# Optimization experiments

Hardware: AMD Instinct MI355X
Metric: run time of the kernel (lower is better)

The kernel has to match this reference:

```python
import jax, jax.numpy as jnp
import numpy as np
import math

B, L, C_IN = 256, 128, 75
D_EMB = 128      # DataEmbedding d_model
D_MODEL = 126    # encoder d_model (= L-2 after ODConv valid conv k=3)
H = 6
D_HEAD = D_MODEL // H  # 21
D_FF = 2048
FACTOR = 5
K_NUM = 4        # ODConv kernel_num (default)
ATT_CH = 16      # max(int(128*0.0625), 16)
EPS = 1e-5


def _ln(x, g, b):
    m = x.mean(-1, keepdims=True)
    v = ((x - m) ** 2).mean(-1, keepdims=True)
    return (x - m) * jax.lax.rsqrt(v + EPS) * g + b


def _bn_eval(x, g, b):
    # eval-mode BatchNorm, running_mean=0 running_var=1
    return x * (g / np.sqrt(1.0 + EPS)) + b


def _conv1d(x, w, b=None):
    out = jax.lax.conv_general_dilated(x, w, (1,), 'VALID',
                                       dimension_numbers=('NCH', 'OIH', 'NCH'))
    if b is not None:
        out = out + b[None, :, None]
    return out


def _pos_embed(n, d):
    pos = np.arange(n)[:, None].astype(np.float32)
    div = np.exp(np.arange(0, d, 2).astype(np.float32) * (-math.log(10000.0) / d))
    pe = np.zeros((n, d), np.float32)
    pe[:, 0::2] = np.sin(pos * div)
    pe[:, 1::2] = np.cos(pos * div)
    return jnp.asarray(pe)


def _prob_attention(Q, K, V, key):
    # Informer ProbAttention, mask_flag=False. Q,K,V: [B,H,Lq,D]
    b, h, lq, d = Q.shape
    lk = K.shape[2]
    u_keys = min(FACTOR * int(np.ceil(np.log(lk))), lk)
    n_top = min(FACTOR * int(np.ceil(np.log(lq))), lq)
    idx = jax.random.randint(key, (lq, u_keys), 0, lk)     # sampled key ids per query
    K_s = K[:, :, idx, :]                                  # [B,H,Lq,u,D]
    qks = jnp.einsum('bhld,bhlud->bhlu', Q, K_s)
    M = qks.max(-1) - qks.sum(-1) / lk                     # sparsity measure
    _, top = jax.lax.top_k(M, n_top)                       # [B,H,n_top]
    Qr = jnp.take_along_axis(Q, top[..., None], axis=2)    # [B,H,n_top,D]
    scores = jnp.einsum('bhud,bhkd->bhuk', Qr, K) / np.sqrt(d).astype(np.float32)
    upd = jnp.einsum('bhuk,bhkd->bhud', jax.nn.softmax(scores, -1), V)
    ctx = jnp.broadcast_to(V.mean(2, keepdims=True), Q.shape)  # initial context
    bi = jnp.arange(b)[:, None, None]
    hi = jnp.arange(h)[None, :, None]
    return ctx.at[bi, hi, top].set(upd)


def _forward(x_enc, x_mark_enc, token_w, time_w, time_b,
             od_fc_w, od_bn_g, od_bn_b, od_ch_w, od_ch_b, od_fil_w, od_fil_b,
             od_sp_w, od_sp_b, od_ker_w, od_ker_b, od_weight,
             q_w, q_b, k_w, k_b, v_w, v_b, o_w, o_b,
             ffn1_w, ffn1_b, ffn2_w, ffn2_b, ln1_g, ln1_b, ln2_g, ln2_b,
             cl_w, cl_b, cl_bn_g, cl_bn_b, enc_ln_g, enc_ln_b, fc_w, fc_b):
    # ---- DataEmbedding (token circular conv + pos + timeF linear; dropout=eval) ----
    xt = jnp.pad(x_enc.transpose(0, 2, 1), ((0, 0), (0, 0), (1, 1)), mode='wrap')
    tok = _conv1d(xt, token_w).transpose(0, 2, 1)          # [B,L,128]
    emb = tok + _pos_embed(L, D_EMB)[None] + (x_mark_enc @ time_w + time_b)

    # ---- ODConv1d(128,128,k=3,pad=0) on [B,128,L] ----
    x = emb.transpose(0, 2, 1)                             # [B,128,L]
    gap = x.mean(-1)                                       # [B,128]
    a = jax.nn.relu(_bn_eval(gap @ od_fc_w, od_bn_g, od_bn_b))   # [B,16]
    ch_att = jax.nn.sigmoid(a @ od_ch_w + od_ch_b)         # [B,128]
    fil_att = jax.nn.sigmoid(a @ od_fil_w + od_fil_b)      # [B,128]
    sp_att = jax.nn.sigmoid(a @ od_sp_w + od_sp_b)         # [B,3]
    ker_att = jax.nn.softmax(a @ od_ker_w + od_ker_b, -1)  # [B,4]
    xc = x * ch_att[:, :, None]
    agg_w = jnp.einsum('bn,bj,noij->boij', ker_att, sp_att, od_weight)  # [B,128,128,3]
    lout = L - 2
    patches = jnp.stack([xc[:, :, j:j + lout] for j in range(3)], axis=2)  # [B,128,3,126]
    x = jnp.einsum('boij,bijt->bot', agg_w, patches) * fil_att[:, :, None]  # [B,128,126]
    # encoder reads this as (seq=128, d_model=126)

    key = jax.random.key(42)

    def enc_layer(xx, i):
        b, l, _ = xx.shape
        Q = (xx @ q_w[i] + q_b[i]).reshape(b, l, H, D_HEAD).transpose(0, 2, 1, 3)
        Kk = (xx @ k_w[i] + k_b[i]).reshape(b, l, H, D_HEAD).transpose(0, 2, 1, 3)
        Vv = (xx @ v_w[i] + v_b[i]).reshape(b, l, H, D_HEAD).transpose(0, 2, 1, 3)
        ctx = _prob_attention(Q, Kk, Vv, jax.random.fold_in(key, i))
        new_x = ctx.transpose(0, 2, 1, 3).reshape(b, l, D_MODEL) @ o_w[i] + o_b[i]
        xx = _ln(xx + new_x, ln1_g[i], ln1_b[i])
        y = jax.nn.gelu(xx @ ffn1_w[i] + ffn1_b[i], approximate=False)
        y = y @ ffn2_w[i] + ffn2_b[i]
        return _ln(xx + y, ln2_g[i], ln2_b[i])

    x = enc_layer(x, 0)
    # ConvLayer distilling: circular conv k3 + BN + ELU + maxpool(k3,s2,p1): 128 -> 64
    xt = jnp.pad(x.transpose(0, 2, 1), ((0, 0), (0, 0), (1, 1)), mode='wrap')
    xt = _conv1d(xt, cl_w, cl_b)
    xt = jax.nn.elu(_bn_eval(xt, cl_bn_g[None, :, None], cl_bn_b[None, :, None]))
    xt = jax.lax.reduce_window(xt, -jnp.inf, jax.lax.max, (1, 1, 3), (1, 1, 2),
                               [(0, 0), (0, 0), (1, 1)])
    x = xt.transpose(0, 2, 1)                              # [B,64,126]
    x = enc_layer(x, 1)
    x = _ln(x, enc_ln_g, enc_ln_b)

    out = x.transpose(0, 2, 1) @ fc_w + fc_b               # [B,126,1]
    return out.transpose(0, 2, 1)                          # [B,1,126]


def setup_inputs() -> dict:
    key = jax.random.key(0)
    it = iter(jax.random.split(key, 48))
    def rn(shape, s=0.05):
        return jax.random.normal(next(it), shape, dtype=jnp.float32) * s
    return {
        'x_enc': jax.random.normal(next(it), (B, L, C_IN), jnp.float32),
        'x_mark_enc': jax.random.uniform(next(it), (B, L, 3), jnp.float32, -0.5, 0.5),
        'token_w': rn((D_EMB, C_IN, 3), 0.1),
        'time_w': rn((3, D_EMB), 0.1), 'time_b': rn((D_EMB,)),
        'od_fc_w': rn((D_EMB, ATT_CH), 0.1),
        'od_bn_g': jnp.ones((ATT_CH,)), 'od_bn_b': jnp.zeros((ATT_CH,)),
        'od_ch_w': rn((ATT_CH, D_EMB), 0.1), 'od_ch_b': rn((D_EMB,)),
        'od_fil_w': rn((ATT_CH, D_EMB), 0.1), 'od_fil_b': rn((D_EMB,)),
        'od_sp_w': rn((ATT_CH, 3), 0.1), 'od_sp_b': rn((3,)),
        'od_ker_w': rn((ATT_CH, K_NUM), 0.1), 'od_ker_b': rn((K_NUM,)),
        'od_weight': rn((K_NUM, D_EMB, D_EMB, 3), 0.05),
        'q_w': rn((2, D_MODEL, D_MODEL)), 'q_b': rn((2, D_MODEL)),
        'k_w': rn((2, D_MODEL, D_MODEL)), 'k_b': rn((2, D_MODEL)),
        'v_w': rn((2, D_MODEL, D_MODEL)), 'v_b': rn((2, D_MODEL)),
        'o_w': rn((2, D_MODEL, D_MODEL)), 'o_b': rn((2, D_MODEL)),
        'ffn1_w': rn((2, D_MODEL, D_FF), 0.03), 'ffn1_b': rn((2, D_FF)),
        'ffn2_w': rn((2, D_FF, D_MODEL), 0.03), 'ffn2_b': rn((2, D_MODEL)),
        'ln1_g': jnp.ones((2, D_MODEL)), 'ln1_b': jnp.zeros((2, D_MODEL)),
        'ln2_g': jnp.ones((2, D_MODEL)), 'ln2_b': jnp.zeros((2, D_MODEL)),
        'cl_w': rn((D_MODEL, D_MODEL, 3), 0.05), 'cl_b': rn((D_MODEL,)),
        'cl_bn_g': jnp.ones((D_MODEL,)), 'cl_bn_b': jnp.zeros((D_MODEL,)),
        'enc_ln_g': jnp.ones((D_MODEL,)), 'enc_ln_b': jnp.zeros((D_MODEL,)),
        'fc_w': rn((L // 2, 1), 0.1), 'fc_b': rn((1,)),
    }


def reference(x_enc, x_mark_enc, token_w, time_w, time_b,
              od_fc_w, od_bn_g, od_bn_b, od_ch_w, od_ch_b, od_fil_w, od_fil_b,
              od_sp_w, od_sp_b, od_ker_w, od_ker_b, od_weight,
              q_w, q_b, k_w, k_b, v_w, v_b, o_w, o_b,
              ffn1_w, ffn1_b, ffn2_w, ffn2_b, ln1_g, ln1_b, ln2_g, ln2_b,
              cl_w, cl_b, cl_bn_g, cl_bn_b, enc_ln_g, enc_ln_b, fc_w, fc_b):
    return _forward(x_enc, x_mark_enc, token_w, time_w, time_b,
                    od_fc_w, od_bn_g, od_bn_b, od_ch_w, od_ch_b, od_fil_w, od_fil_b,
                    od_sp_w, od_sp_b, od_ker_w, od_ker_b, od_weight,
                    q_w, q_b, k_w, k_b, v_w, v_b, o_w, o_b,
                    ffn1_w, ffn1_b, ffn2_w, ffn2_b, ln1_g, ln1_b, ln2_g, ln2_b,
                    cl_w, cl_b, cl_bn_g, cl_bn_b, enc_ln_g, enc_ln_b, fc_w, fc_b)
```

## Files before the change

### kernel.cpp

```cpp
#include <hip/hip_runtime.h>
#include <math.h>

#define NB 256
#define DM 126
#define DE 128
#define NH 6
#define DHd 21
#define DFF 2048
#define CIN 75
#define L0 128
#define NTOP 25

#ifndef IDX_MODE
#define IDX_MODE 0
#endif

typedef const float* fp;
typedef unsigned short u16;
typedef short s8v __attribute__((ext_vector_type(8)));
typedef float f4v __attribute__((ext_vector_type(4)));

__device__ __forceinline__ u16 f2bf(float x){
  unsigned u = __float_as_uint(x);
  unsigned r = (u + 0x7FFFu + ((u >> 16) & 1u)) >> 16;
  return (u16)r;
}
__device__ __forceinline__ float bf2f(u16 v){
  unsigned uu = ((unsigned)v) << 16;
  return __uint_as_float(uu);
}

__device__ __forceinline__ void gld_lds16(const u16* g, u16* l){
  __builtin_amdgcn_global_load_lds((const __attribute__((address_space(1))) unsigned int*)(const void*)g,
                                   (__attribute__((address_space(3))) unsigned int*)(void*)l,
                                   16, 0, 0);
}

__device__ __forceinline__ unsigned cvt_pk_bf16(float lo, float hi){
  unsigned r;
  asm("v_cvt_pk_bf16_f32 %0, %1, %2" : "=v"(r) : "v"(lo), "v"(hi));
  return r;
}

__device__ __forceinline__ void tf2(unsigned k0, unsigned k1, unsigned x0, unsigned x1,
                                    unsigned &o0, unsigned &o1){
  unsigned ks2 = k0 ^ k1 ^ 0x1BD11BDAu;
  x0 += k0; x1 += k1;
  #define RR(r) { x0 += x1; x1 = (x1 << (r)) | (x1 >> (32 - (r))); x1 ^= x0; }
  RR(13) RR(15) RR(26) RR(6)
  x0 += k1;  x1 += ks2 + 1u;
  RR(17) RR(29) RR(16) RR(24)
  x0 += ks2; x1 += k0 + 2u;
  RR(13) RR(15) RR(26) RR(6)
  x0 += k0;  x1 += k1 + 3u;
  RR(17) RR(29) RR(16) RR(24)
  x0 += k1;  x1 += ks2 + 4u;
  RR(13) RR(15) RR(26) RR(6)
  x0 += ks2; x1 += k0 + 5u;
  #undef RR
  o0 = x0; o1 = x1;
}

__global__ __launch_bounds__(256) void k_zero(float* out, int n){
  int i = blockIdx.x*256 + threadIdx.x;
  if (i < n) out[i] = 0.f;
}

__global__ __launch_bounds__(256) void k_idx(int* idx0, int* idx1){
  int tid = threadIdx.x;
  unsigned a0,a1,c0,c1;
  tf2(0u,42u, 0u,0u, a0,a1);
  tf2(0u,42u, 0u,1u, c0,c1);
  for (int f = tid; f < 3200; f += 256){
    unsigned y0,y1;
#if IDX_MODE==0
    tf2(a0,a1, 0u, (unsigned)(3200+f), y0,y1); idx0[f] = (int)(y1 & 127u);
#elif IDX_MODE==1
    tf2(a0,a1, 0u, (unsigned)(3200+f), y0,y1); idx0[f] = (int)(y0 & 127u);
#elif IDX_MODE==2
    tf2(a0,a1, (unsigned)f, (unsigned)(3200+f), y0,y1); idx0[f] = (int)(y1 & 127u);
#else
    tf2(a0,a1, (unsigned)f, (unsigned)(3200+f), y0,y1); idx0[f] = (int)(y0 & 127u);
#endif
  }
  for (int f = tid; f < 1600; f += 256){
    unsigned y0,y1;
#if IDX_MODE==0
    tf2(c0,c1, 0u, (unsigned)(1600+f), y0,y1); idx1[f] = (int)(y1 & 63u);
#elif IDX_MODE==1
    tf2(c0,c1, 0u, (unsigned)(1600+f), y0,y1); idx1[f] = (int)(y0 & 63u);
#elif IDX_MODE==2
    tf2(c0,c1, (unsigned)f, (unsigned)(1600+f), y0,y1); idx1[f] = (int)(y1 & 63u);
#else
    tf2(c0,c1, (unsigned)f, (unsigned)(1600+f), y0,y1); idx1[f] = (int)(y0 & 63u);
#endif
  }
}

__global__ __launch_bounds__(256) void k_wprep(fp token_w, fp clw,
                                               fp qw, fp qb, fp kw, fp kb, fp vw, fp vb, fp ow,
                                               u16* wemb, u16* wdist, u16* wqkv, u16* wo,
                                               float* qbias){
  int i = blockIdx.x*256 + threadIdx.x;
  if (i < 32768){
    int n = i >> 8, k = i & 255;
    float v = 0.f;
    if (k < 225){ int q = k/75, c = k - q*75; v = token_w[(size_t)n*225 + c*3 + q]; }
    wemb[i] = f2bf(v);
    return;
  }
  i -= 32768;
  if (i < 49152){
    int n = i / 384, k = i - n*384;
    float v = 0.f;
    if (n < DM && k < 378){ int q = k/126, ci = k - q*126; v = clw[((size_t)n*DM + ci)*3 + q]; }
    wdist[i] = f2bf(v);
    return;
  }
  i -= 49152;
  if (i < 2*49152){
    int layer = i / 49152, jj = i - layer*49152;
    int n = jj >> 7, k = jj & 127;
    int sec = n >> 7, nn = n & 127;
    const float* w = (sec == 0) ? qw : ((sec == 1) ? kw : vw);
    float v = (nn < DM && k < DM) ? w[((size_t)layer*DM + k)*DM + nn] : 0.f;
    wqkv[(size_t)layer*49152 + jj] = f2bf(v);
    return;
  }
  i -= 2*49152;
  if (i < 2*16384){
    int layer = i / 16384, jj = i - layer*16384;
    int n = jj >> 7, k = jj & 127;
    float v = (n < DM && k < DM) ? ow[(size_t)layer*DM*DM + k*DM + n] : 0.f;
    wo[(size_t)layer*16384 + jj] = f2bf(v);
    return;
  }
  i -= 2*16384;
  if (i < 768){
    int layer = i / 384, n = i - layer*384;
    int sec = n >> 7, nn = n & 127;
    const float* bp = (sec == 0) ? qb : ((sec == 1) ? kb : vb);
    qbias[(size_t)layer*384 + n] = (nn < DM) ? bp[layer*DM + nn] : 0.f;
  }
}

__global__ __launch_bounds__(256) void k_wtrans(fp f1w, fp f2w, u16* w1t, u16* w2t){
  __shared__ u16 sT[64*65];
  const int t = blockIdx.x;
  const int tid = threadIdx.x, lane = tid & 63, rg = tid >> 6;
  if (t < 128){
    int layer = t >> 6, rem = t & 63;
    int kt = rem >> 5, nt = rem & 31;
    #pragma unroll
    for (int rr = 0; rr < 16; rr++){
      int row = rg + rr*4;
      int k = kt*64 + row;
      float v = (k < DM) ? f1w[((size_t)layer*DM + k)*DFF + nt*64 + lane] : 0.f;
      sT[row*65 + lane] = f2bf(v);
    }
    __syncthreads();
    #pragma unroll
    for (int rr = 0; rr < 16; rr++){
      int nrow = rg + rr*4;
      int n_glob = nt*64 + nrow;
      w1t[(size_t)layer*262144 + (size_t)n_glob*128 + kt*64 + lane] = sT[lane*65 + nrow];
    }
  } else {
    int t2 = t - 128;
    int layer = t2 >> 6, rem = t2 & 63;
    int nt = rem >> 5, ft = rem & 31;
    #pragma unroll
    for (int rr = 0; rr < 16; rr++){
      int row = rg + rr*4;
      int f = ft*64 + row;
      int n = nt*64 + lane;
      float v = (n < DM) ? f2w[((size_t)layer*DFF + f)*DM + n] : 0.f;
      sT[row*65 + lane] = f2bf(v);
    }
    __syncthreads();
    #pragma unroll
    for (int rr = 0; rr < 16; rr++){
      int nrow = rg + rr*4;
      int n_glob = nt*64 + nrow;
      w2t[(size_t)layer*262144 + (size_t)n_glob*2048 + ft*64 + lane] = sT[lane*65 + nrow];
    }
  }
}

__global__ __launch_bounds__(256) void k_front(fp x_enc, fp x_mark, const u16* wemb,
                                               fp time_w, fp time_b,
                                               fp fcw, fp bng, fp bnb,
                                               fp chw, fp chb, fp filw, fp filb,
                                               fp spw, fp spb, fp kerw, fp kerb,
                                               fp odw, float* xout){
  __shared__ __align__(16) u16 smem[71232];
  u16*   sXT = smem;
  u16*   sW  = smem + 17680;
  u16*   sA  = smem + 17680;
  float* sE  = reinterpret_cast<float*>(smem + 17680);
  float* red = reinterpret_cast<float*>(smem + 69904);
  float* gap = reinterpret_cast<float*>(smem + 70416);
  float* aAct= reinterpret_cast<float*>(smem + 70672);
  float* sch = reinterpret_cast<float*>(smem + 70704);
  float* sfil= reinterpret_cast<float*>(smem + 70960);
  float* ssp = reinterpret_cast<float*>(smem + 71216);
  float* sker= reinterpret_cast<float*>(smem + 71224);
  const int tid = threadIdx.x;
  const int wave = tid >> 6, lane = tid & 63, quad = lane >> 4, l15 = lane & 15;
  const int b = blockIdx.x;
  const f4v z4 = {0.f,0.f,0.f,0.f};
  const int mBase = wave * 32;

  {
    const float4* xb = reinterpret_cast<const float4*>(x_enc + (size_t)b*L0*CIN);
    for (int p4 = tid; p4 < (L0*CIN)/4; p4 += 256){
      float4 v4 = xb[p4];
      float vv[4] = {v4.x, v4.y, v4.z, v4.w};
      int e0 = p4*4;
      #pragma unroll
      for (int j = 0; j < 4; j++){
        int e = e0 + j;
        int sr = e / CIN, c = e - sr*CIN;
        u16 bv = f2bf(vv[j]);
        sA[((sr + 1) & 127)*264 + c] = bv;
        sA[sr*264 + 75 + c] = bv;
        sA[((sr + 127) & 127)*264 + 150 + c] = bv;
      }
    }
    for (int p = tid; p < 128*31; p += 256){
      int row = p / 31, c2 = p - row*31;
      sA[row*264 + 225 + c2] = 0;
    }
  }
  __syncthreads();
  {
    f4v acc[2][8];
    #pragma unroll
    for (int m = 0; m < 2; m++)
      #pragma unroll
      for (int t = 0; t < 8; t++) acc[m][t] = z4;
    for (int ks = 0; ks < 8; ks++){
      s8v a0 = *reinterpret_cast<const s8v*>(sA + (mBase + l15)*264 + ks*32 + quad*8);
      s8v a1 = *reinterpret_cast<const s8v*>(sA + (mBase + 16 + l15)*264 + ks*32 + quad*8);
      const u16* wb = wemb + (size_t)l15*256 + ks*32 + quad*8;
      #pragma unroll
      for (int t = 0; t < 8; t++){
        s8v bfr = *reinterpret_cast<const s8v*>(wb + (size_t)t*16*256);
        acc[0][t] = __builtin_amdgcn_mfma_f32_16x16x32_bf16(a0, bfr, acc[0][t], 0, 0, 0);
        acc[1][t] = __builtin_amdgcn_mfma_f32_16x16x32_bf16(a1, bfr, acc[1][t], 0, 0, 0);
      }
    }
    float divc[8], tw0c[8], tw1c[8], tw2c[8], tbc[8];
    #pragma unroll
    for (int t = 0; t < 8; t++){
      int col = t*16 + l15;
      int i2 = col >> 1;
      divc[t] = __expf((float)(2*i2) * (-9.210340371976184f / 128.f));
      tw0c[t] = time_w[col]; tw1c[t] = time_w[128 + col]; tw2c[t] = time_w[256 + col];
      tbc[t] = time_b[col];
    }
    #pragma unroll
    for (int m = 0; m < 2; m++){
      #pragma unroll
      for (int r = 0; r < 4; r++){
        int row = mBase + m*16 + quad*4 + r;
        const float* mk = x_mark + ((size_t)b*L0 + row)*3;
        float m0v = mk[0], m1v = mk[1], m2v = mk[2];
        #pragma unroll
        for (int t = 0; t < 8; t++){
          int col = t*16 + l15;
          float ang = (float)row * divc[t];
          float pe = (col & 1) ? __cosf(ang) : __sinf(ang);
          float tm = m0v*tw0c[t] + m1v*tw1c[t] + m2v*tw2c[t] + tbc[t];
          sE[row*132 + col] = acc[m][t][r] + pe + tm;
        }
      }
    }
  }
  __syncthreads();
  {
    int col = tid & 127, half = tid >> 7;
    float s = 0.f;
    for (int r = 0; r < 64; r++) s += sE[(half*64 + r)*132 + col];
    red[tid] = s;
  }
  __syncthreads();
  if (tid < 128) gap[tid] = (red[tid] + red[tid + 128]) * (1.f/128.f);
  __syncthreads();
  if (tid < 16){
    float acc = 0.f;
    for (int e = 0; e < DE; e++) acc += gap[e]*fcw[e*16 + tid];
    acc = acc * (bng[tid] / sqrtf(1.f + 1e-5f)) + bnb[tid];
    aAct[tid] = fmaxf(acc, 0.f);
  }
  __syncthreads();
  if (tid < 128){
    float accc = 0.f, accf = 0.f;
    for (int c = 0; c < 16; c++){ accc += aAct[c]*chw[c*DE + tid]; accf += aAct[c]*filw[c*DE + tid]; }
    sch[tid]  = 1.f/(1.f + __expf(-(accc + chb[tid])));
    sfil[tid] = 1.f/(1.f + __expf(-(accf + filb[tid])));
  } else if (tid < 131){
    int t = tid - 128;
    float acc = 0.f;
    for (int c = 0; c < 16; c++) acc += aAct[c]*spw[c*3 + t];
    ssp[t] = 1.f/(1.f + __expf(-(acc + spb[t])));
  } else if (tid == 132){
    float v[4]; float mx = -1e30f;
    for (int n = 0; n < 4; n++){
      float acc = 0.f;
      for (int c = 0; c < 16; c++) acc += aAct[c]*kerw[c*4 + n];
      v[n] = acc + kerb[n]; mx = fmaxf(mx, v[n]);
    }
    float ss = 0.f;
    for (int n = 0; n < 4; n++){ v[n] = __expf(v[n]-mx); ss += v[n]; }
    for (int n = 0; n < 4; n++) sker[n] = v[n]/ss;
  }
  __syncthreads();
  for (int p = tid; p < 130*128; p += 256){
    int l = p >> 7, i = p & 127;
    float v = (l < 128) ? sE[l*132 + i]*sch[i] : 0.f;
    sXT[l*136 + i] = f2bf(v);
  }
  __syncthreads();
  {
    float kr0 = sker[0], kr1 = sker[1], kr2 = sker[2], kr3 = sker[3];
    float spq[3]; spq[0] = ssp[0]; spq[1] = ssp[1]; spq[2] = ssp[2];
    const float4* od4 = (const float4*)odw;
    for (int p4 = tid; p4 < 128*384/4; p4 += 256){
      float4 w0 = od4[p4];
      float4 w1 = od4[12288 + p4];
      float4 w2 = od4[24576 + p4];
      float4 w3 = od4[36864 + p4];
      float vv[4] = { kr0*w0.x + kr1*w1.x + kr2*w2.x + kr3*w3.x,
                      kr0*w0.y + kr1*w1.y + kr2*w2.y + kr3*w3.y,
                      kr0*w0.z + kr1*w1.z + kr2*w2.z + kr3*w3.z,
                      kr0*w0.w + kr1*w1.w + kr2*w2.w + kr3*w3.w };
      int e0 = p4*4;
      #pragma unroll
      for (int j = 0; j < 4; j++){
        int e = e0 + j;
        int o = e / 384, rem = e - o*384;
        int i = rem / 3, q = rem - i*3;
        sW[(q*128 + o)*136 + i] = f2bf(vv[j] * spq[q]);
      }
    }
  }
  __syncthreads();
  {
    f4v acc[2][8];
    #pragma unroll
    for (int m = 0; m < 2; m++)
      #pragma unroll
      for (int t = 0; t < 8; t++) acc[m][t] = z4;
    for (int q = 0; q < 3; q++){
      const u16* wq = sW + q*128*136;
      #pragma unroll
      for (int ks = 0; ks < 4; ks++){
        s8v a0 = *reinterpret_cast<const s8v*>(wq + (mBase + l15)*136 + ks*32 + quad*8);
        s8v a1 = *reinterpret_cast<const s8v*>(wq + (mBase + 16 + l15)*136 + ks*32 + quad*8);
        #pragma unroll
        for (int t = 0; t < 8; t++){
          s8v bfr = *reinterpret_cast<const s8v*>(sXT + (t*16 + l15 + q)*136 + ks*32 + quad*8);
          acc[0][t] = __builtin_amdgcn_mfma_f32_16x16x32_bf16(a0, bfr, acc[0][t], 0, 0, 0);
          acc[1][t] = __builtin_amdgcn_mfma_f32_16x16x32_bf16(a1, bfr, acc[1][t], 0, 0, 0);
        }
      }
    }
    #pragma unroll
    for (int t = 0; t < 8; t++){
      int tt = t*16 + l15;
      if (tt < DM){
        #pragma unroll
        for (int m = 0; m < 2; m++){
          #pragma unroll
          for (int r = 0; r < 4; r++){
            int o = mBase + m*16 + quad*4 + r;
            xout[((size_t)b*DE + o)*DM + tt] = sfil[o] * acc[m][t][r];
          }
        }
      }
    }
  }
}

__global__ __launch_bounds__(256) void k_qkv_mfma(const float* xin, const u16* wqkv,
                                                  const float* qkvb, float* qkv,
                                                  float* vt, int L, int lshift, int lmask){
  __shared__ __align__(16) u16 sX[64*136];
  const int tid = threadIdx.x;
  const int wave = tid >> 6, lane = tid & 63, quad = lane >> 4, l15 = lane & 15;
  const size_t rows0 = (size_t)blockIdx.x * 64;
  for (int p = tid; p < 64*128; p += 256){
    int r = p >> 7, c = p & 127;
    float v = (c < DM) ? xin[(rows0 + r)*DM + c] : 0.f;
    sX[r*136 + c] = f2bf(v);
  }
  __syncthreads();
  const f4v z4 = {0.f,0.f,0.f,0.f};
  f4v acc[24];
  #pragma unroll
  for (int t = 0; t < 24; t++) acc[t] = z4;
  const int m0 = wave * 16;
  #pragma unroll
  for (int ks = 0; ks < 4; ks++){
    s8v a = *reinterpret_cast<const s8v*>(sX + (m0 + l15)*136 + ks*32 + quad*8);
    const u16* wb = wqkv + (size_t)l15*128 + ks*32 + quad*8;
    #pragma unroll
    for (int t = 0; t < 24; t++){
      s8v b = *reinterpret_cast<const s8v*>(wb + (size_t)t*16*128);
      acc[t] = __builtin_amdgcn_mfma_f32_16x16x32_bf16(a, b, acc[t], 0, 0, 0);
    }
  }
  #pragma unroll
  for (int t = 0; t < 24; t++){
    int col = t*16 + l15;
    float bv = qkvb[col];
    if (col < 256){
      #pragma unroll
      for (int r = 0; r < 4; r++){
        int row = m0 + quad*4 + r;
        qkv[(rows0 + row)*256 + col] = acc[t][r] + bv;
      }
    } else {
      int c = col - 256;
      if (c < DM){
        int h = c / DHd, d = c - h*DHd;
        #pragma unroll
        for (int r = 0; r < 4; r++){
          int gr = (int)rows0 + m0 + quad*4 + r;
          int b = gr >> lshift, l = gr & lmask;
          vt[((size_t)(b*NH + h)*DHd + d)*L + l] = acc[t][r] + bv;
        }
      }
    }
  }
}

__global__ __launch_bounds__(128) void k_attn(const float* qkv, const float* vt,
                                              const int* idx, int L,
                                              int* posmap, float* vmean, float* upd){
  __shared__ __align__(16) float sK[2816];
  __shared__ int sTop[32];
  const int tid = threadIdx.x;
  const int wave = tid >> 6, lane = tid & 63, quad = lane >> 4, l15 = lane & 15;
  const int bh = blockIdx.x;
  const int b = bh / NH, h = bh - b*NH;
  float* sM = sK + 2688;
  u16* sPb = reinterpret_cast<u16*>(sK);
  const float* qbase = qkv + (size_t)(b*L)*256 + h*DHd;
  const float* vb = vt + (size_t)bh*DHd*L;
  const f4v z4 = {0.f,0.f,0.f,0.f};
  const int ntn = L >> 4;
  const int d0 = quad*8;
  const int mt = wave;

  for (int p = tid; p < L*DHd; p += 128){
    int l = p / DHd, d = p - l*DHd;
    sK[p] = qbase[(size_t)l*256 + 128 + d];
  }
  posmap[bh*L0 + tid] = -1;
  __syncthreads();
  if (tid < L){
    const int l = tid;
    const float* qg = qbase + (size_t)l*256;
    float qr[DHd];
    #pragma unroll
    for (int d = 0; d < DHd; d++) qr[d] = qg[d];
    float mx = -1e30f, sm = 0.f;
    #pragma unroll
    for (int u = 0; u < NTOP; u++){
      int kk = idx[l*NTOP + u];
      const float* kp = sK + kk*DHd;
      float acc = 0.f;
      #pragma unroll
      for (int d = 0; d < DHd; d++) acc += qr[d]*kp[d];
      mx = fmaxf(mx, acc); sm += acc;
    }
    sM[l] = mx - sm/(float)L;
  }
  __syncthreads();
  if (wave == 0){
    for (int it = 0; it < NTOP; it++){
      float bv = sM[lane]; int bi = lane;
      if (L == 128){
        float v1 = sM[lane + 64];
        if (v1 > bv){ bv = v1; bi = lane + 64; }
      }
      #pragma unroll
      for (int off = 32; off > 0; off >>= 1){
        float ov = __shfl_xor(bv, off);
        int   oi = __shfl_xor(bi, off);
        if (ov > bv || (ov == bv && oi < bi)){ bv = ov; bi = oi; }
      }
      if (lane == 0){
        sM[bi] = -1e30f;
        posmap[bh*L0 + bi] = it;
        sTop[it] = bi;
      }
    }
  }
  __syncthreads();

  s8v aq;
  {
    int uu = mt*16 + l15; if (uu >= NTOP) uu = 0;
    int r = sTop[uu];
    const float* qp = qbase + (size_t)r*256 + d0;
    #pragma unroll
    for (int j = 0; j < 8; j++) aq[j] = (short)f2bf(qp[j]);
  }
  f4v sc[8];
  for (int nt = 0; nt < ntn; nt++){
    const float* kp = sK + (size_t)(nt*16 + l15)*DHd + d0;
    s8v bb;
    #pragma unroll
    for (int j = 0; j < 8; j++) bb[j] = (d0 + j < DHd) ? (short)f2bf(kp[j]) : (short)0;
    sc[nt] = __builtin_amdgcn_mfma_f32_16x16x32_bf16(aq, bb, z4, 0, 0, 0);
  }
  __syncthreads();
  const float inv21 = 0.21821789023599236f;
  #pragma unroll
  for (int r4 = 0; r4 < 4; r4++){
    float mx = -1e30f;
    for (int nt = 0; nt < ntn; nt++) mx = fmaxf(mx, sc[nt][r4]*inv21);
    #pragma unroll
    for (int off = 1; off < 16; off <<= 1) mx = fmaxf(mx, __shfl_xor(mx, off));
    float e[8]; float ss = 0.f;
    for (int nt = 0; nt < ntn; nt++){ e[nt] = __expf(sc[nt][r4]*inv21 - mx); ss += e[nt]; }
    #pragma unroll
    for (int off = 1; off < 16; off <<= 1) ss += __shfl_xor(ss, off);
    float dn = 1.f / ss;
    int u = mt*16 + quad*4 + r4;
    for (int nt = 0; nt < ntn; nt++)
      sPb[u*136 + nt*16 + l15] = f2bf(e[nt]*dn);
  }
  if (wave == 1){
    u16 invL = f2bf(1.f/(float)L);
    for (int c = lane; c < L; c += 64) sPb[25*136 + c] = invL;
  }
  f4v pv[2];
  pv[0] = z4; pv[1] = z4;
  int kSteps = L >> 5;
  for (int ks = 0; ks < kSteps; ks++){
    #pragma unroll
    for (int nt = 0; nt < 2; nt++){
      int d = nt*16 + l15;
      s8v bb;
      if (d < DHd){
        const float* vp = vb + (size_t)d*L + ks*32 + d0;
        #pragma unroll
        for (int j = 0; j < 8; j++) bb[j] = (short)f2bf(vp[j]);
      } else {
        #pragma unroll
        for (int j = 0; j < 8; j++) bb[j] = (short)0;
      }
      s8v a = *reinterpret_cast<const s8v*>(sPb + (mt*16 + l15)*136 + ks*32 + d0);
      pv[nt] = __builtin_amdgcn_mfma_f32_16x16x32_bf16(a, bb, pv[nt], 0, 0, 0);
    }
  }
  #pragma unroll
  for (int nt = 0; nt < 2; nt++){
    #pragma unroll
    for (int r4 = 0; r4 < 4; r4++){
      int u = mt*16 + quad*4 + r4;
      int d = nt*16 + l15;
      if (d < DHd){
        if (u < NTOP)       upd[((size_t)bh*NTOP + u)*DHd + d] = pv[nt][r4];
        else if (u == NTOP) vmean[bh*DHd + d] = pv[nt][r4];
      }
    }
  }
}

__global__ __launch_bounds__(256) void k_oproj_mfma(const float* xin, const float* vmean,
                                                    const int* posmap, const float* upd,
                                                    const u16* wo, fp ob, fp g, fp bb,
                                                    int layer, int lshift, int lmask, float* xmid){
  __shared__ __align__(16) float sOf[64*129];
  __shared__ float prs[128];
  __shared__ float smean[64], srstd[64];
  u16* sX = reinterpret_cast<u16*>(sOf);
  const int tid = threadIdx.x;
  const int wave = tid >> 6, lane = tid & 63, quad = lane >> 4, l15 = lane & 15;
  const int m0 = wave * 16;
  const size_t rows0 = (size_t)blockIdx.x * 64;
  for (int p = tid; p < 64*128; p += 256){
    int r = p >> 7, c = p & 127;
    int gr = (int)rows0 + r, b = gr >> lshift, l = gr & lmask;
    float v = 0.f;
    if (c < DM){
      int h = c / DHd, d = c - h*DHd;
      int bh = b*NH + h;
      int pos = posmap[bh*L0 + l];
      v = (pos >= 0) ? upd[((size_t)bh*NTOP + pos)*DHd + d] : vmean[bh*DHd + d];
    }
    sX[r*136 + c] = f2bf(v);
  }
  __syncthreads();
  const f4v z4 = {0.f,0.f,0.f,0.f};
  f4v acc[8];
  #pragma unroll
  for (int t = 0; t < 8; t++) acc[t] = z4;
  #pragma unroll
  for (int ks = 0; ks < 4; ks++){
    s8v a = *reinterpret_cast<const s8v*>(sX + (m0 + l15)*136 + ks*32 + quad*8);
    const u16* wb = wo + (size_t)l15*128 + ks*32 + quad*8;
    #pragma unroll
    for (int t = 0; t < 8; t++){
      s8v b = *reinterpret_cast<const s8v*>(wb + (size_t)t*16*128);
      acc[t] = __builtin_amdgcn_mfma_f32_16x16x32_bf16(a, b, acc[t], 0, 0, 0);
    }
  }
  __syncthreads();
  #pragma unroll
  for (int t = 0; t < 8; t++){
    int col = t*16 + l15;
    #pragma unroll
    for (int r = 0; r < 4; r++){
      sOf[(m0 + quad*4 + r)*129 + col] = acc[t][r];
    }
  }
  __syncthreads();
  const float* obl = ob + (size_t)layer*DM;
  for (int p = tid; p < 64*DM; p += 256){
    int r = p / DM, c = p - r*DM;
    sOf[r*129 + c] += xin[(rows0 + r)*DM + c] + obl[c];
  }
  __syncthreads();
  if (tid < 128){
    int row = tid >> 1, half = tid & 1;
    float s = 0.f;
    for (int c = half*63; c < half*63 + 63; c++) s += sOf[row*129 + c];
    prs[tid] = s;
  }
  __syncthreads();
  if (tid < 128 && (tid & 1) == 0) smean[tid>>1] = (prs[tid] + prs[tid+1]) / (float)DM;
  __syncthreads();
  if (tid < 128){
    int row = tid >> 1, half = tid & 1;
    float mn = smean[row];
    float s = 0.f;
    for (int c = half*63; c < half*63 + 63; c++){ float d = sOf[row*129 + c] - mn; s += d*d; }
    prs[tid] = s;
  }
  __syncthreads();
  if (tid < 128 && (tid & 1) == 0) srstd[tid>>1] = rsqrtf((prs[tid] + prs[tid+1])/(float)DM + 1e-5f);
  __syncthreads();
  const float* gl = g  + (size_t)layer*DM;
  const float* bl = bb + (size_t)layer*DM;
  for (int p = tid; p < 64*DM; p += 256){
    int r = p / DM, c = p - r*DM;
    xmid[(rows0 + r)*DM + c] = (sOf[r*129 + c] - smean[r])*srstd[r]*gl[c] + bl[c];
  }
}

__device__ __forceinline__ float gelu_fast(float x){
  float x2 = x*x;
  float u = x * __builtin_fmaf(0.10295128f, x2, 2.30212056f);
  u = fminf(u, 126.f);
#if __has_builtin(__builtin_amdgcn_exp2f)
  float t = __builtin_amdgcn_exp2f(u);
#else
  float t = __expf(u * 0.69314718056f);
#endif
  return x * t * __builtin_amdgcn_rcpf(t + 1.f);
}


__device__ __forceinline__ void stage_w1_p(const u16* w1t, int j, u16* buf, int p){
  int n = p >> 4, c = p & 15;
  int cg = c ^ (n & 7);
  gld_lds16(w1t + (((size_t)(j*64 + n)) << 7) + cg*8,
            buf + (size_t)((p >> 6) << 6)*8);
}
__device__ __forceinline__ void stage_w2_p(const u16* w2t, int j, u16* buf, int p){
  int n = p >> 3, c = p & 7;
  int cg = c ^ (n & 7);
  gld_lds16(w2t + (size_t)n*2048 + j*64 + cg*8,
            buf + (size_t)((p >> 6) << 6)*8);
}

__device__ __forceinline__ int yaddr(int row, int col){
  return row*64 + (((col >> 3) ^ (row & 7)) << 3) + (col & 7);
}

__device__ __forceinline__ void lgkm_barrier(){
  asm volatile("s_waitcnt lgkmcnt(0)" ::: "memory");
  __builtin_amdgcn_sched_barrier(0);
  __builtin_amdgcn_s_barrier();
  __builtin_amdgcn_sched_barrier(0);
}

template<int NT>
__global__ __launch_bounds__(NT) void k_ffn(const float* xmid, const u16* w1t, const u16* w2t,
                                            fp b1, fp b2w, fp g, fp bb, int layer, float* xout){
  constexpr int ROWS = NT/8;
  constexpr int NMG  = NT/256;
  constexpr int SYG  = NMG*2048;
  constexpr int SP   = 1024/NT;
  __shared__ __align__(16) u16 smem[SYG + 4*8192];
  __shared__ float prs[2*ROWS];
  __shared__ float smean[ROWS], srstd[ROWS];
  u16* wA0 = smem + SYG;
  u16* wA1 = wA0 + 8192;
  u16* wB0 = wA1 + 8192;
  u16* wB1 = wB0 + 8192;
  const int tid  = threadIdx.x;
  const int wave = tid >> 6, lane = tid & 63, quad = lane >> 4, l15 = lane & 15;
  const int mg = wave >> 2, ng = wave & 3;
  const int rowb = mg * 32;
  u16* sYg = smem + mg*2048;
  const size_t rows0 = (size_t)blockIdx.x * ROWS;

  s8v aX[2][4];
  #pragma unroll
  for (int mt = 0; mt < 2; mt++){
    const float* xr = xmid + (rows0 + rowb + mt*16 + l15)*(size_t)DM;
    #pragma unroll
    for (int ks = 0; ks < 4; ks++){
      #pragma unroll
      for (int j = 0; j < 8; j++){
        int c = ks*32 + quad*8 + j;
        float v = (c < DM) ? xr[c] : 0.f;
        aX[mt][ks][j] = (short)f2bf(v);
      }
    }
  }
  #pragma unroll
  for (int r = 0; r < SP; r++){
    stage_w1_p(w1t, 0, wA0, r*NT + tid);
    stage_w2_p(w2t, 0, wB0, r*NT + tid);
  }

  const float* b1l = b1 + (size_t)layer*DFF;
  const f4v z4 = {0.f, 0.f, 0.f, 0.f};
  f4v acc2[2][2];
  acc2[0][0]=z4; acc2[0][1]=z4; acc2[1][0]=z4; acc2[1][1]=z4;

  for (int j = 0; j < 32; j++){
    u16* wAcur = (j & 1) ? wA1 : wA0;
    u16* wAnxt = (j & 1) ? wA0 : wA1;
    u16* wBcur = (j & 1) ? wB1 : wB0;
    u16* wBnxt = (j & 1) ? wB0 : wB1;
    __syncthreads();
    if (j < 31){
      #pragma unroll
      for (int r = 0; r < SP; r++){
        stage_w1_p(w1t, j+1, wAnxt, r*NT + tid);
        stage_w2_p(w2t, j+1, wBnxt, r*NT + tid);
      }
    }
    f4v acc1[2];
    acc1[0] = z4; acc1[1] = z4;
    {
      int nloc = ng*16 + l15;
      #pragma unroll
      for (int ks = 0; ks < 4; ks++){
        int cg = (ks*4 + quad) ^ (nloc & 7);
        s8v b = *reinterpret_cast<const s8v*>(wAcur + nloc*128 + cg*8);
        acc1[0] = __builtin_amdgcn_mfma_f32_16x16x32_bf16(aX[0][ks], b, acc1[0], 0, 0, 0);
        acc1[1] = __builtin_amdgcn_mfma_f32_16x16x32_bf16(aX[1][ks], b, acc1[1], 0, 0, 0);
      }
    }
    {
      int col = ng*16 + l15;
      float bv = b1l[j*64 + col];
      #pragma unroll
      for (int mt = 0; mt < 2; mt++){
        float y0 = gelu_fast(acc1[mt][0] + bv);
        float y1 = gelu_fast(acc1[mt][1] + bv);
        float y2 = gelu_fast(acc1[mt][2] + bv);
        float y3 = gelu_fast(acc1[mt][3] + bv);
        unsigned p01 = cvt_pk_bf16(y0, y1);
        unsigned p23 = cvt_pk_bf16(y2, y3);
        int r0 = mt*16 + quad*4;
        sYg[yaddr(r0,     col)] = (u16)p01;
        sYg[yaddr(r0 + 1, col)] = (u16)(p01 >> 16);
        sYg[yaddr(r0 + 2, col)] = (u16)p23;
        sYg[yaddr(r0 + 3, col)] = (u16)(p23 >> 16);
      }
    }
    lgkm_barrier();
    #pragma unroll
    for (int ks2 = 0; ks2 < 2; ks2++){
      int ga = ((ks2*4 + quad) ^ (l15 & 7)) << 3;
      s8v a0 = *reinterpret_cast<const s8v*>(sYg + (l15)*64 + ga);
      s8v a1 = *reinterpret_cast<const s8v*>(sYg + (16 + l15)*64 + ga);
      #pragma unroll
      for (int t = 0; t < 2; t++){
        int nloc = ng*32 + t*16 + l15;
        int cg = (ks2*4 + quad) ^ (nloc & 7);
        s8v b = *reinterpret_cast<const s8v*>(wBcur + nloc*64 + cg*8);
        acc2[0][t] = __builtin_amdgcn_mfma_f32_16x16x32_bf16(a0, b, acc2[0][t], 0, 0, 0);
        acc2[1][t] = __builtin_amdgcn_mfma_f32_16x16x32_bf16(a1, b, acc2[1][t], 0, 0, 0);
      }
    }
  }

  __syncthreads();
  float* sO = reinterpret_cast<float*>(smem);
  #pragma unroll
  for (int mt = 0; mt < 2; mt++)
    #pragma unroll
    for (int t = 0; t < 2; t++)
      #pragma unroll
      for (int r = 0; r < 4; r++)
        sO[(rowb + mt*16 + quad*4 + r)*129 + ng*32 + t*16 + l15] = acc2[mt][t][r];
  __syncthreads();
  const float* b2l = b2w + (size_t)layer*DM;
  for (int p = tid; p < ROWS*DM; p += NT){
    int r = p / DM, c = p - r*DM;
    sO[r*129 + c] += b2l[c] + xmid[(rows0 + r)*DM + c];
  }
  __syncthreads();
  if (tid < 2*ROWS){
    int row = tid >> 1, half = tid & 1;
    float s = 0.f;
    for (int c = half*63; c < half*63 + 63; c++) s += sO[row*129 + c];
    prs[tid] = s;
  }
  __syncthreads();
  if (tid < 2*ROWS && (tid & 1) == 0) smean[tid>>1] = (prs[tid] + prs[tid+1]) / (float)DM;
  __syncthreads();
  if (tid < 2*ROWS){
    int row = tid >> 1, half = tid & 1;
    float mn = smean[row];
    float s = 0.f;
    for (int c = half*63; c < half*63 + 63; c++){ float d = sO[row*129 + c] - mn; s += d*d; }
    prs[tid] = s;
  }
  __syncthreads();
  if (tid < 2*ROWS && (tid & 1) == 0) srstd[tid>>1] = rsqrtf((prs[tid] + prs[tid+1])/(float)DM + 1e-5f);
  __syncthreads();
  const float* gl = g  + (size_t)layer*DM;
  const float* bl = bb + (size_t)layer*DM;
  for (int p = tid; p < ROWS*DM; p += NT){
    int r = p / DM, c = p - r*DM;
    xout[(rows0 + r)*DM + c] = (sO[r*129 + c] - smean[r])*srstd[r]*gl[c] + bl[c];
  }
}

__global__ __launch_bounds__(256) void k_distill_mfma(const float* xin, const u16* wdist,
                                                      fp clb, fp bng, fp bnb, float* xout){
  __shared__ __align__(16) u16 sA[128*392];
  const int tid = threadIdx.x;
  const int wave = tid >> 6, lane = tid & 63, quad = lane >> 4, l15 = lane & 15;
  const int b = blockIdx.x;
  {
    const float4* xb = reinterpret_cast<const float4*>(xin + (size_t)b*128*DM);
    for (int p4 = tid; p4 < (128*DM)/4; p4 += 256){
      float4 v4 = xb[p4];
      float vv[4] = {v4.x, v4.y, v4.z, v4.w};
      int e0 = p4*4;
      #pragma unroll
      for (int j = 0; j < 4; j++){
        int e = e0 + j;
        int sr = e / DM, ci = e - sr*DM;
        u16 bv = f2bf(vv[j]);
        sA[((sr + 1) & 127)*392 + ci] = bv;
        sA[sr*392 + 126 + ci] = bv;
        sA[((sr + 127) & 127)*392 + 252 + ci] = bv;
      }
    }
    for (int p = tid; p < 128*6; p += 256){
      int row = p / 6, c2 = p - row*6;
      sA[row*392 + 378 + c2] = 0;
    }
  }
  __syncthreads();
  const f4v z4 = {0.f,0.f,0.f,0.f};
  f4v acc[2][8];
  #pragma unroll
  for (int m = 0; m < 2; m++)
    #pragma unroll
    for (int t = 0; t < 8; t++) acc[m][t] = z4;
  const int mBase = wave * 32;
  for (int ks = 0; ks < 12; ks++){
    s8v a0 = *reinterpret_cast<const s8v*>(sA + (mBase + l15)*392 + ks*32 + quad*8);
    s8v a1 = *reinterpret_cast<const s8v*>(sA + (mBase + 16 + l15)*392 + ks*32 + quad*8);
    const u16* wb = wdist + (size_t)l15*384 + ks*32 + quad*8;
    #pragma unroll
    for (int t = 0; t < 8; t++){
      s8v bfr = *reinterpret_cast<const s8v*>(wb + (size_t)t*16*384);
      acc[0][t] = __builtin_amdgcn_mfma_f32_16x16x32_bf16(a0, bfr, acc[0][t], 0, 0, 0);
      acc[1][t] = __builtin_amdgcn_mfma_f32_16x16x32_bf16(a1, bfr, acc[1][t], 0, 0, 0);
    }
  }
  __syncthreads();
  float* zsh = reinterpret_cast<float*>(sA);
  const float bnscale = 1.f / sqrtf(1.f + 1e-5f);
  #pragma unroll
  for (int t = 0; t < 8; t++){
    int co = t*16 + l15;
    if (co < DM){
      float cb = clb[co];
      float gg = bng[co] * bnscale, bv = bnb[co];
      #pragma unroll
      for (int m = 0; m < 2; m++){
        #pragma unroll
        for (int r = 0; r < 4; r++){
          int row = mBase + m*16 + quad*4 + r;
          float z = (acc[m][t][r] + cb)*gg + bv;
          z = (z > 0.f) ? z : (__expf(z) - 1.f);
          zsh[row*130 + co] = z;
        }
      }
    }
  }
  __syncthreads();
  for (int p = tid; p < 64*DM; p += 256){
    int j = p / DM, co = p - j*DM;
    float best = zsh[(2*j)*130 + co];
    if (j > 0) best = fmaxf(best, zsh[(2*j - 1)*130 + co]);
    best = fmaxf(best, zsh[(2*j + 1)*130 + co]);
    xout[((size_t)b*64 + j)*DM + co] = best;
  }
}

__global__ __launch_bounds__(128) void k_final(const float* xin, fp g, fp bb,
                                               fp fcw, fp fcb, float* out){
  __shared__ float xs[64][DM];
  __shared__ float mean_s[64], rstd_s[64];
  int b = blockIdx.x, t = threadIdx.x;
  for (int p = t; p < 64*DM; p += 128){ xs[p/DM][p%DM] = xin[(size_t)b*64*DM + p]; }
  __syncthreads();
  if (t < 64){
    float s = 0.f;
    for (int m = 0; m < DM; m++) s += xs[t][m];
    float mn = s / (float)DM;
    float v = 0.f;
    for (int m = 0; m < DM; m++){ float d = xs[t][m] - mn; v += d*d; }
    mean_s[t] = mn; rstd_s[t] = rsqrtf(v / (float)DM + 1e-5f);
  }
  __syncthreads();
  if (t < DM){
    float gv = g[t], bv = bb[t];
    float acc = fcb[0];
    for (int l = 0; l < 64; l++){
      float xn = (xs[l][t] - mean_s[l])*rstd_s[l]*gv + bv;
      acc += xn * fcw[l];
    }
    out[b*DM + t] = acc;
  }
}

extern "C" void kernel_launch(void* const* d_in, const int* in_sizes, int n_in,
                              void* d_out, int out_size, void* d_ws, size_t ws_size,
                              hipStream_t stream) {
  fp x_enc   = (fp)d_in[0];
  fp x_mark  = (fp)d_in[1];
  fp token_w = (fp)d_in[2];
  fp time_w  = (fp)d_in[3];
  fp time_b  = (fp)d_in[4];
  fp od_fc_w = (fp)d_in[5];
  fp od_bn_g = (fp)d_in[6];
  fp od_bn_b = (fp)d_in[7];
  fp od_ch_w = (fp)d_in[8];
  fp od_ch_b = (fp)d_in[9];
  fp od_fil_w= (fp)d_in[10];
  fp od_fil_b= (fp)d_in[11];
  fp od_sp_w = (fp)d_in[12];
  fp od_sp_b = (fp)d_in[13];
  fp od_ker_w= (fp)d_in[14];
  fp od_ker_b= (fp)d_in[15];
  fp od_wt   = (fp)d_in[16];
  fp q_w = (fp)d_in[17]; fp q_b = (fp)d_in[18];
  fp k_w = (fp)d_in[19]; fp k_b = (fp)d_in[20];
  fp v_w = (fp)d_in[21]; fp v_b = (fp)d_in[22];
  fp o_w = (fp)d_in[23]; fp o_b = (fp)d_in[24];
  fp f1w = (fp)d_in[25]; fp f1b = (fp)d_in[26];
  fp f2w = (fp)d_in[27]; fp f2b = (fp)d_in[28];
  fp ln1g= (fp)d_in[29]; fp ln1b= (fp)d_in[30];
  fp ln2g= (fp)d_in[31]; fp ln2b= (fp)d_in[32];
  fp cl_w= (fp)d_in[33]; fp cl_b= (fp)d_in[34];
  fp clbg= (fp)d_in[35]; fp clbb= (fp)d_in[36];
  fp elng= (fp)d_in[37]; fp elnb= (fp)d_in[38];
  fp fc_w= (fp)d_in[39]; fp fc_b= (fp)d_in[40];

  const size_t OFF_IDX0 = 0;
  const size_t OFF_IDX1 = OFF_IDX0 + 3200;
  const size_t OFF_CH   = OFF_IDX1 + 1600;
  const size_t OFF_FIL  = OFF_CH  + (size_t)NB*DE;
  const size_t OFF_SP   = OFF_FIL + (size_t)NB*DE;
  const size_t OFF_KER  = OFF_SP  + (size_t)NB*4;
  const size_t OFF_VM   = OFF_KER + (size_t)NB*4;
  const size_t OFF_POS  = OFF_VM  + (size_t)NB*NH*DHd;
  const size_t OFF_UPD  = OFF_POS + (size_t)NB*NH*L0;
  const size_t OFF_STOP = OFF_UPD + (size_t)NB*NH*NTOP*DHd;
  const size_t OFF_WTS  = (OFF_STOP + (size_t)NB*NH*NTOP + 255) & ~(size_t)255;
  const size_t WTS_FLOATS = (2*262144 + 2*262144 + 2*49152 + 2*16384 + 49152 + 32768)/2 + 2*384;
  const size_t OFF_BIG  = (OFF_WTS + WTS_FLOATS + 255) & ~(size_t)255;
  const size_t SBUF     = (size_t)NB*DE*L0;
  const size_t TOTAL    = OFF_BIG + 4*SBUF;

  if (ws_size < TOTAL*sizeof(float)){
    hipLaunchKernelGGL(k_zero, dim3((out_size+255)/256), dim3(256), 0, stream,
                       (float*)d_out, out_size);
    return;
  }

  float* ws = (float*)d_ws;
  int* idx0 = (int*)(ws + OFF_IDX0);
  int* idx1 = (int*)(ws + OFF_IDX1);
  float* vme = ws + OFF_VM;
  int* posm  = (int*)(ws + OFF_POS);
  float* updb= ws + OFF_UPD;
  u16* w1tb  = (u16*)(ws + OFF_WTS);
  u16* w2tb  = w1tb + 2*262144;
  u16* wqkvb = w2tb + 2*262144;
  u16* wob   = wqkvb + 2*49152;
  u16* wdistb= wob + 2*16384;
  u16* wembb = wdistb + 49152;
  float* qkvbias = (float*)(wembb + 32768);

  float* X    = ws + OFF_BIG;
  float* QKV  = X + SBUF;
  float* VT   = X + 3*SBUF;
  float* xmid = QKV;
  float* ffno = QKV + SBUF;

  hipLaunchKernelGGL(k_idx, dim3(1), dim3(256), 0, stream, idx0, idx1);
  hipLaunchKernelGGL(k_wprep, dim3(835), dim3(256), 0, stream,
                     token_w, cl_w, q_w, q_b, k_w, k_b, v_w, v_b, o_w,
                     wembb, wdistb, wqkvb, wob, qkvbias);
  hipLaunchKernelGGL(k_wtrans, dim3(256), dim3(256), 0, stream,
                     f1w, f2w, w1tb, w2tb);
  hipLaunchKernelGGL(k_front, dim3(NB), dim3(256), 0, stream,
                     x_enc, x_mark, wembb, time_w, time_b,
                     od_fc_w, od_bn_g, od_bn_b, od_ch_w, od_ch_b, od_fil_w, od_fil_b,
                     od_sp_w, od_sp_b, od_ker_w, od_ker_b, od_wt, X);

  hipLaunchKernelGGL(k_qkv_mfma, dim3(NB*L0/64), dim3(256), 0, stream,
                     X, wqkvb, qkvbias, QKV, VT, 128, 7, 127);
  hipLaunchKernelGGL(k_attn, dim3(NB*NH), dim3(128), 0, stream,
                     QKV, VT, idx0, L0, posm, vme, updb);
  hipLaunchKernelGGL(k_oproj_mfma, dim3(NB*L0/64), dim3(256), 0, stream,
                     X, vme, posm, updb, wob, o_b, ln1g, ln1b, 0, 7, 127, xmid);
  hipLaunchKernelGGL((k_ffn<1024>), dim3(NB*L0/128), dim3(1024), 0, stream,
                     xmid, w1tb, w2tb, f1b, f2b, ln2g, ln2b, 0, ffno);

  hipLaunchKernelGGL(k_distill_mfma, dim3(NB), dim3(256), 0, stream,
                     ffno, wdistb, cl_b, clbg, clbb, X);

  hipLaunchKernelGGL(k_qkv_mfma, dim3(NB*64/64), dim3(256), 0, stream,
                     X, wqkvb + 49152, qkvbias + 384, QKV, VT, 64, 6, 63);
  hipLaunchKernelGGL(k_attn, dim3(NB*NH), dim3(128), 0, stream,
                     QKV, VT, idx1, 64, posm, vme, updb);
  hipLaunchKernelGGL(k_oproj_mfma, dim3(NB*64/64), dim3(256), 0, stream,
                     X, vme, posm, updb, wob + 16384, o_b, ln1g, ln1b, 1, 6, 63, xmid);
  hipLaunchKernelGGL((k_ffn<512>), dim3(NB*64/64), dim3(512), 0, stream,
                     xmid, w1tb + 262144, w2tb + 262144, f1b, f2b, ln2g, ln2b, 1, ffno);

  hipLaunchKernelGGL(k_final, dim3(NB), dim3(128), 0, stream,
                     ffno, elng, elnb, fc_w, fc_b, (float*)d_out);
  (void)in_sizes; (void)n_in; (void)out_size; (void)ws_size;
}
```

Baseline: 608.3 us.

## Fuse distill conv into layer-0 FFN and final LN/FC into layer-1 FFN

Each FFN kernel instance now handles one batch item and runs the next stage in its epilogue. Layer 0 runs the distilling conv, BN, ELU and maxpool from shared memory, and layer 1 runs the final encoder LayerNorm and the FC projection. This removes two kernel launches and the global-memory round trip of the FFN outputs. In exchange the layer-0 FFN shared-memory buffer is enlarged to hold the conv im2col tile, which may lower occupancy, and the epilogues add extra barriers.

After: 592.2 us. 1.03x faster.

```diff
diff --git a/kernel.cpp b/kernel.cpp
--- a/kernel.cpp
+++ b/kernel.cpp
@@ -693,12 +693,15 @@
 
 template<int NT>
 __global__ __launch_bounds__(NT) void k_ffn(const float* xmid, const u16* w1t, const u16* w2t,
-                                            fp b1, fp b2w, fp g, fp bb, int layer, float* xout){
+                                            fp b1, fp b2w, fp g, fp bb, int layer,
+                                            const u16* wdist, fp e1, fp e2, fp e3, fp e4,
+                                            float* out2){
   constexpr int ROWS = NT/8;
   constexpr int NMG  = NT/256;
   constexpr int SYG  = NMG*2048;
   constexpr int SP   = 1024/NT;
-  __shared__ __align__(16) u16 smem[SYG + 4*8192];
+  constexpr int SMEMU = (NT == 1024) ? 128*392 : (SYG + 4*8192);
+  __shared__ __align__(16) u16 smem[SMEMU];
   __shared__ float prs[2*ROWS];
   __shared__ float smean[ROWS], srstd[ROWS];
   u16* wA0 = smem + SYG;
@@ -834,113 +837,105 @@
   __syncthreads();
   const float* gl = g  + (size_t)layer*DM;
   const float* bl = bb + (size_t)layer*DM;
-  for (int p = tid; p < ROWS*DM; p += NT){
-    int r = p / DM, c = p - r*DM;
-    xout[(rows0 + r)*DM + c] = (sO[r*129 + c] - smean[r])*srstd[r]*gl[c] + bl[c];
-  }
-}
-
-__global__ __launch_bounds__(256) void k_distill_mfma(const float* xin, const u16* wdist,
-                                                      fp clb, fp bng, fp bnb, float* xout){
-  __shared__ __align__(16) u16 sA[128*392];
-  const int tid = threadIdx.x;
-  const int wave = tid >> 6, lane = tid & 63, quad = lane >> 4, l15 = lane & 15;
-  const int b = blockIdx.x;
-  {
-    const float4* xb = reinterpret_cast<const float4*>(xin + (size_t)b*128*DM);
-    for (int p4 = tid; p4 < (128*DM)/4; p4 += 256){
-      float4 v4 = xb[p4];
-      float vv[4] = {v4.x, v4.y, v4.z, v4.w};
-      int e0 = p4*4;
-      #pragma unroll
-      for (int j = 0; j < 4; j++){
-        int e = e0 + j;
-        int sr = e / DM, ci = e - sr*DM;
-        u16 bv = f2bf(vv[j]);
-        sA[((sr + 1) & 127)*392 + ci] = bv;
-        sA[sr*392 + 126 + ci] = bv;
-        sA[((sr + 127) & 127)*392 + 252 + ci] = bv;
-      }
-    }
-    for (int p = tid; p < 128*6; p += 256){
-      int row = p / 6, c2 = p - row*6;
-      sA[row*392 + 378 + c2] = 0;
-    }
-  }
-  __syncthreads();
-  const f4v z4 = {0.f,0.f,0.f,0.f};
-  f4v acc[2][8];
-  #pragma unroll
-  for (int m = 0; m < 2; m++)
-    #pragma unroll
-    for (int t = 0; t < 8; t++) acc[m][t] = z4;
-  const int mBase = wave * 32;
-  for (int ks = 0; ks < 12; ks++){
-    s8v a0 = *reinterpret_cast<const s8v*>(sA + (mBase + l15)*392 + ks*32 + quad*8);
-    s8v a1 = *reinterpret_cast<const s8v*>(sA + (mBase + 16 + l15)*392 + ks*32 + quad*8);
-    const u16* wb = wdist + (size_t)l15*384 + ks*32 + quad*8;
-    #pragma unroll
-    for (int t = 0; t < 8; t++){
-      s8v bfr = *reinterpret_cast<const s8v*>(wb + (size_t)t*16*384);
-      acc[0][t] = __builtin_amdgcn_mfma_f32_16x16x32_bf16(a0, bfr, acc[0][t], 0, 0, 0);
-      acc[1][t] = __builtin_amdgcn_mfma_f32_16x16x32_bf16(a1, bfr, acc[1][t], 0, 0, 0);
-    }
-  }
-  __syncthreads();
-  float* zsh = reinterpret_cast<float*>(sA);
-  const float bnscale = 1.f / sqrtf(1.f + 1e-5f);
-  #pragma unroll
-  for (int t = 0; t < 8; t++){
-    int co = t*16 + l15;
-    if (co < DM){
-      float cb = clb[co];
-      float gg = bng[co] * bnscale, bv = bnb[co];
-      #pragma unroll
-      for (int m = 0; m < 2; m++){
+
+  if constexpr (NT == 1024){
+    float rv[16];
+    #pragma unroll
+    for (int k = 0; k < 16; k++){
+      int p = tid + k*1024;
+      if (p < 128*DM){
+        int r = p / DM, c = p - r*DM;
+        rv[k] = (sO[r*129 + c] - smean[r])*srstd[r]*gl[c] + bl[c];
+      } else rv[k] = 0.f;
+    }
+    __syncthreads();
+    u16* sAd = smem;
+    #pragma unroll
+    for (int k = 0; k < 16; k++){
+      int p = tid + k*1024;
+      if (p < 128*DM){
+        int r = p / DM, c = p - r*DM;
+        u16 bv = f2bf(rv[k]);
+        sAd[((r + 1) & 127)*392 + c] = bv;
+        sAd[r*392 + 126 + c] = bv;
+        sAd[((r + 127) & 127)*392 + 252 + c] = bv;
+      }
+    }
+    if (tid < 768){ int row = tid / 6, c2 = tid - row*6; sAd[row*392 + 378 + c2] = 0; }
+    __syncthreads();
+    const int mrow  = (wave & 7) * 16;
+    const int tbase = (wave >> 3) * 4;
+    f4v dac[4];
+    dac[0]=z4; dac[1]=z4; dac[2]=z4; dac[3]=z4;
+    for (int ks = 0; ks < 12; ks++){
+      s8v a = *reinterpret_cast<const s8v*>(sAd + (mrow + l15)*392 + ks*32 + quad*8);
+      const u16* wbp = wdist + (size_t)l15*384 + ks*32 + quad*8;
+      #pragma unroll
+      for (int t = 0; t < 4; t++){
+        s8v bfr = *reinterpret_cast<const s8v*>(wbp + (size_t)(tbase + t)*16*384);
+        dac[t] = __builtin_amdgcn_mfma_f32_16x16x32_bf16(a, bfr, dac[t], 0, 0, 0);
+      }
+    }
+    __syncthreads();
+    float* zsh = reinterpret_cast<float*>(smem);
+    const float bnscale = 1.f / sqrtf(1.f + 1e-5f);
+    #pragma unroll
+    for (int t = 0; t < 4; t++){
+      int co = (tbase + t)*16 + l15;
+      if (co < DM){
+        float cb = e1[co];
+        float gg = e2[co] * bnscale, bv = e3[co];
         #pragma unroll
         for (int r = 0; r < 4; r++){
-          int row = mBase + m*16 + quad*4 + r;
-          float z = (acc[m][t][r] + cb)*gg + bv;
+          int row = mrow + quad*4 + r;
+          float z = (dac[t][r] + cb)*gg + bv;
           z = (z > 0.f) ? z : (__expf(z) - 1.f);
           zsh[row*130 + co] = z;
         }
       }
     }
-  }
-  __syncthreads();
-  for (int p = tid; p < 64*DM; p += 256){
-    int j = p / DM, co = p - j*DM;
-    float best = zsh[(2*j)*130 + co];
-    if (j > 0) best = fmaxf(best, zsh[(2*j - 1)*130 + co]);
-    best = fmaxf(best, zsh[(2*j + 1)*130 + co]);
-    xout[((size_t)b*64 + j)*DM + co] = best;
-  }
-}
-
-__global__ __launch_bounds__(128) void k_final(const float* xin, fp g, fp bb,
-                                               fp fcw, fp fcb, float* out){
-  __shared__ float xs[64][DM];
-  __shared__ float mean_s[64], rstd_s[64];
-  int b = blockIdx.x, t = threadIdx.x;
-  for (int p = t; p < 64*DM; p += 128){ xs[p/DM][p%DM] = xin[(size_t)b*64*DM + p]; }
-  __syncthreads();
-  if (t < 64){
-    float s = 0.f;
-    for (int m = 0; m < DM; m++) s += xs[t][m];
-    float mn = s / (float)DM;
-    float v = 0.f;
-    for (int m = 0; m < DM; m++){ float d = xs[t][m] - mn; v += d*d; }
-    mean_s[t] = mn; rstd_s[t] = rsqrtf(v / (float)DM + 1e-5f);
-  }
-  __syncthreads();
-  if (t < DM){
-    float gv = g[t], bv = bb[t];
-    float acc = fcb[0];
-    for (int l = 0; l < 64; l++){
-      float xn = (xs[l][t] - mean_s[l])*rstd_s[l]*gv + bv;
-      acc += xn * fcw[l];
-    }
-    out[b*DM + t] = acc;
+    __syncthreads();
+    for (int p = tid; p < 64*DM; p += 1024){
+      int jj = p / DM, co = p - jj*DM;
+      float best = zsh[(2*jj)*130 + co];
+      if (jj > 0) best = fmaxf(best, zsh[(2*jj - 1)*130 + co]);
+      best = fmaxf(best, zsh[(2*jj + 1)*130 + co]);
+      out2[((size_t)blockIdx.x*64 + jj)*DM + co] = best;
+    }
+  } else {
+    for (int p = tid; p < ROWS*DM; p += NT){
+      int r = p / DM, c = p - r*DM;
+      sO[r*129 + c] = (sO[r*129 + c] - smean[r])*srstd[r]*gl[c] + bl[c];
+    }
+    __syncthreads();
+    if (tid < 2*ROWS){
+      int row = tid >> 1, half = tid & 1;
+      float s = 0.f;
+      for (int c = half*63; c < half*63 + 63; c++) s += sO[row*129 + c];
+      prs[tid] = s;
+    }
+    __syncthreads();
+    if (tid < 2*ROWS && (tid & 1) == 0) smean[tid>>1] = (prs[tid] + prs[tid+1]) / (float)DM;
+    __syncthreads();
+    if (tid < 2*ROWS){
+      int row = tid >> 1, half = tid & 1;
+      float mn = smean[row];
+      float s = 0.f;
+      for (int c = half*63; c < half*63 + 63; c++){ float d = sO[row*129 + c] - mn; s += d*d; }
+      prs[tid] = s;
+    }
+    __syncthreads();
+    if (tid < 2*ROWS && (tid & 1) == 0) srstd[tid>>1] = rsqrtf((prs[tid] + prs[tid+1])/(float)DM + 1e-5f);
+    __syncthreads();
+    if (tid < DM){
+      float gv = e1[tid], bv2 = e2[tid];
+      float acc = e4[0];
+      for (int l = 0; l < 64; l++){
+        float xn = (sO[l*129 + tid] - smean[l])*srstd[l]*gv + bv2;
+        acc += xn * e3[l];
+      }
+      out2[(size_t)blockIdx.x*DM + tid] = acc;
+    }
   }
 }
 
@@ -1017,7 +1012,6 @@
   float* QKV  = X + SBUF;
   float* VT   = X + 3*SBUF;
   float* xmid = QKV;
-  float* ffno = QKV + SBUF;
 
   hipLaunchKernelGGL(k_idx, dim3(1), dim3(256), 0, stream, idx0, idx1);
   hipLaunchKernelGGL(k_wprep, dim3(835), dim3(256), 0, stream,
@@ -1036,11 +1030,9 @@
                      QKV, VT, idx0, L0, posm, vme, updb);
   hipLaunchKernelGGL(k_oproj_mfma, dim3(NB*L0/64), dim3(256), 0, stream,
                      X, vme, posm, updb, wob, o_b, ln1g, ln1b, 0, 7, 127, xmid);
-  hipLaunchKernelGGL((k_ffn<1024>), dim3(NB*L0/128), dim3(1024), 0, stream,
-                     xmid, w1tb, w2tb, f1b, f2b, ln2g, ln2b, 0, ffno);
-
-  hipLaunchKernelGGL(k_distill_mfma, dim3(NB), dim3(256), 0, stream,
-                     ffno, wdistb, cl_b, clbg, clbb, X);
+  hipLaunchKernelGGL((k_ffn<1024>), dim3(NB), dim3(1024), 0, stream,
+                     xmid, w1tb, w2tb, f1b, f2b, ln2g, ln2b, 0,
+                     wdistb, cl_b, clbg, clbb, cl_b, X);
 
   hipLaunchKernelGGL(k_qkv_mfma, dim3(NB*64/64), dim3(256), 0, stream,
                      X, wqkvb + 49152, qkvbias + 384, QKV, VT, 64, 6, 63);
@@ -1048,10 +1040,8 @@
                      QKV, VT, idx1, 64, posm, vme, updb);
   hipLaunchKernelGGL(k_oproj_mfma, dim3(NB*64/64), dim3(256), 0, stream,
                      X, vme, posm, updb, wob + 16384, o_b, ln1g, ln1b, 1, 6, 63, xmid);
-  hipLaunchKernelGGL((k_ffn<512>), dim3(NB*64/64), dim3(512), 0, stream,
-                     xmid, w1tb + 262144, w2tb + 262144, f1b, f2b, ln2g, ln2b, 1, ffno);
-
-  hipLaunchKernelGGL(k_final, dim3(NB), dim3(128), 0, stream,
-                     ffno, elng, elnb, fc_w, fc_b, (float*)d_out);
+  hipLaunchKernelGGL((k_ffn<512>), dim3(256), dim3(512), 0, stream,
+                     xmid, w1tb + 262144, w2tb + 262144, f1b, f2b, ln2g, ln2b, 1,
+                     wdistb, elng, elnb, fc_w, fc_b, (float*)d_out);
   (void)in_sizes; (void)n_in; (void)out_size; (void)ws_size;
 }
```
